# Performance work log

Hardware: AMD Instinct MI355X
Metric: run time of the kernel (lower is better)

The kernel has to match this reference:

```python
import jax, jax.numpy as jnp
import numpy as np

N_NODES = 100000
N_EDGES = 1600000
D_IN = 256
D_OUT = 256


def _init_linear(key, out_f, in_f):
    # torch nn.Linear default: U(-1/sqrt(in_f), 1/sqrt(in_f))
    kw, kb = jax.random.split(key)
    bound = 1.0 / np.sqrt(in_f)
    W = jax.random.uniform(kw, (out_f, in_f), jnp.float32, -bound, bound)
    b = jax.random.uniform(kb, (out_f,), jnp.float32, -bound, bound)
    return W, b


def setup_inputs() -> dict:
    key = jax.random.key(0)
    ks = jax.random.split(key, 7)
    x = jax.random.normal(ks[0], (N_NODES, D_IN), jnp.float32)
    edge_index = jax.random.randint(ks[1], (2, N_EDGES), 0, N_NODES, jnp.int64)
    W1, b1 = _init_linear(ks[2], D_OUT, D_IN)
    W2, b2 = _init_linear(ks[3], D_OUT // 2, D_OUT)
    W3, b3 = _init_linear(ks[4], D_OUT // 2, D_OUT)
    Wd1, bd1 = _init_linear(ks[5], D_OUT, D_OUT)
    Wd2, bd2 = _init_linear(ks[6], 1, D_OUT)
    return {"x": x, "edge_index": edge_index,
            "W1": W1, "b1": b1, "W2": W2, "b2": b2, "W3": W3, "b3": b3,
            "Wd1": Wd1, "bd1": bd1, "Wd2": Wd2, "bd2": bd2}


def _l2norm(x):
    return x / jnp.linalg.norm(x, axis=-1, keepdims=True)


def reference(x, edge_index, W1, b1, W2, b2, W3, b3, Wd1, bd1, Wd2, bd2):
    src, dst = edge_index[0], edge_index[1]  # source_to_target flow
    x = jax.nn.relu(x @ W1.T + b1)           # [N, D_OUT]
    x = _l2norm(x)
    for _ in range(2):
        # sum-aggregate neighbor messages: scatter-add x[src] into dst
        nm = jax.ops.segment_sum(x[src], dst, num_segments=N_NODES)  # [N, D_OUT]
        x = jax.nn.relu(jnp.concatenate([x @ W2.T + b2, nm @ W3.T + b3], axis=-1))
        x = _l2norm(x)
    x = jax.nn.relu(x @ Wd1.T + bd1)
    return x @ Wd2.T + bd2                    # [N, 1]
```

## Files before the change

kernel.cpp:

```cpp
#include <hip/hip_runtime.h>
#include <math.h>


typedef _Float16 f16x8 __attribute__((ext_vector_type(8)));
typedef float    f32x16 __attribute__((ext_vector_type(16)));

constexpr int DIM = 256;
constexpr int BM  = 128;
constexpr int BK  = 32;
constexpr int SA  = 40;
constexpr int SW  = 40;
constexpr int NBMAX = 392;

__device__ __forceinline__ unsigned pk_hi2(float a, float b) {
    unsigned short ha = __builtin_bit_cast(unsigned short, (_Float16)a);
    unsigned short hb = __builtin_bit_cast(unsigned short, (_Float16)b);
    return (unsigned)ha | ((unsigned)hb << 16);
}
__device__ __forceinline__ unsigned pk_lo2(float a, float b) {
    _Float16 ha = (_Float16)a, hb = (_Float16)b;
    unsigned short la = __builtin_bit_cast(unsigned short, (_Float16)(a - (float)ha));
    unsigned short lb = __builtin_bit_cast(unsigned short, (_Float16)(b - (float)hb));
    return (unsigned)la | ((unsigned)lb << 16);
}
__device__ __forceinline__ unsigned pack_pair(float v) {
    _Float16 hi = (_Float16)v;
    _Float16 lo = (_Float16)(v - (float)hi);
    return (unsigned)__builtin_bit_cast(unsigned short, hi)
         | ((unsigned)__builtin_bit_cast(unsigned short, lo) << 16);
}

template <int AMODE, int EPI>
__device__ __forceinline__
void gemm_body(const void* __restrict__ Av,
               const float* __restrict__ WA, const float* __restrict__ WB,
               const float* __restrict__ bA, const float* __restrict__ bB,
               void* __restrict__ outv,
               const float* __restrict__ wd2, const float* __restrict__ bd2,
               float* __restrict__ out1, int M)
{
    __shared__ __align__(16) _Float16 smem[30720];
    _Float16* As_hi = smem;
    _Float16* As_lo = smem + 5120;
    _Float16* Ws_hi = smem + 10240;
    _Float16* Ws_lo = smem + 20480;

    const int tid  = threadIdx.x;
    const int lane = tid & 63;
    const int w    = tid >> 6;
    const int rh   = w >> 1;
    const int ch   = w & 1;
    const int l31  = lane & 31;
    const int lh   = lane >> 5;
    const int bm0  = blockIdx.x * BM;

    const unsigned* Au = (const unsigned*)Av;
    const int srow = tid >> 3;
    const int sch  = (tid & 7) * 4;

    uint4  pa[4];
    float4 pw[8];

    auto fetchA = [&](int t) {
        const int k0 = t * BK;
        #pragma unroll
        for (int i = 0; i < 4; ++i) {
            const int gr = bm0 + srow + 32 * i;
            uint4 v = {0u, 0u, 0u, 0u};
            if (gr < M) v = *(const uint4*)&Au[(size_t)gr * 256 + k0 + sch];
            pa[i] = v;
        }
    };
    auto fetchW = [&](int t) {
        const int k0 = t * BK;
        #pragma unroll
        for (int i = 0; i < 8; ++i) {
            const int r = srow + 32 * i;
            const float* src = (r < 128) ? &WA[(size_t)r * 256]
                                         : &WB[(size_t)(r - 128) * 256];
            pw[i] = *(const float4*)&src[k0 + sch];
        }
    };
    auto stageA = [&]() {
        #pragma unroll
        for (int i = 0; i < 4; ++i) {
            const int r = srow + 32 * i;
            unsigned h0, h1, l0, l1;
            if (AMODE == 0) {
                const float x0 = __builtin_bit_cast(float, pa[i].x);
                const float x1 = __builtin_bit_cast(float, pa[i].y);
                const float x2 = __builtin_bit_cast(float, pa[i].z);
                const float x3 = __builtin_bit_cast(float, pa[i].w);
                h0 = pk_hi2(x0, x1); h1 = pk_hi2(x2, x3);
                l0 = pk_lo2(x0, x1); l1 = pk_lo2(x2, x3);
            } else {
                h0 = __builtin_amdgcn_perm(pa[i].y, pa[i].x, 0x05040100u);
                l0 = __builtin_amdgcn_perm(pa[i].y, pa[i].x, 0x07060302u);
                h1 = __builtin_amdgcn_perm(pa[i].w, pa[i].z, 0x05040100u);
                l1 = __builtin_amdgcn_perm(pa[i].w, pa[i].z, 0x07060302u);
            }
            uint2 th; th.x = h0; th.y = h1;
            uint2 tl; tl.x = l0; tl.y = l1;
            *(uint2*)&As_hi[r * SA + sch] = th;
            *(uint2*)&As_lo[r * SA + sch] = tl;
        }
    };
    auto stageW = [&]() {
        #pragma unroll
        for (int i = 0; i < 8; ++i) {
            const int r = srow + 32 * i;
            uint2 th; th.x = pk_hi2(pw[i].x, pw[i].y); th.y = pk_hi2(pw[i].z, pw[i].w);
            uint2 tl; tl.x = pk_lo2(pw[i].x, pw[i].y); tl.y = pk_lo2(pw[i].z, pw[i].w);
            *(uint2*)&Ws_hi[r * SW + sch] = th;
            *(uint2*)&Ws_lo[r * SW + sch] = tl;
        }
    };

    f32x16 acc[2][4];
    #pragma unroll
    for (int tr = 0; tr < 2; ++tr)
        #pragma unroll
        for (int tc = 0; tc < 4; ++tc)
            #pragma unroll
            for (int i = 0; i < 16; ++i) acc[tr][tc][i] = 0.0f;

    fetchA(0); fetchW(0);

    #pragma unroll 1
    for (int t = 0; t < DIM / BK; ++t) {
        stageA(); stageW();
        __syncthreads();
        if (t < DIM / BK - 1) { fetchA(t + 1); fetchW(t + 1); }

        #pragma unroll
        for (int ks = 0; ks < 2; ++ks) {
            f16x8 ah[2], al[2], wh[4], wl[4];
            #pragma unroll
            for (int tr = 0; tr < 2; ++tr) {
                const int off = (rh * 64 + tr * 32 + l31) * SA + ks * 16 + lh * 8;
                ah[tr] = *(const f16x8*)&As_hi[off];
                al[tr] = *(const f16x8*)&As_lo[off];
            }
            #pragma unroll
            for (int tc = 0; tc < 4; ++tc) {
                const int off = (ch * 128 + tc * 32 + l31) * SW + ks * 16 + lh * 8;
                wh[tc] = *(const f16x8*)&Ws_hi[off];
                wl[tc] = *(const f16x8*)&Ws_lo[off];
            }
            #pragma unroll
            for (int tr = 0; tr < 2; ++tr)
                #pragma unroll
                for (int tc = 0; tc < 4; ++tc) {
                    acc[tr][tc] = __builtin_amdgcn_mfma_f32_32x32x16_f16(ah[tr], wh[tc], acc[tr][tc], 0, 0, 0);
                    acc[tr][tc] = __builtin_amdgcn_mfma_f32_32x32x16_f16(ah[tr], wl[tc], acc[tr][tc], 0, 0, 0);
                    acc[tr][tc] = __builtin_amdgcn_mfma_f32_32x32x16_f16(al[tr], wh[tc], acc[tr][tc], 0, 0, 0);
                }
        }
        __syncthreads();
    }


    if (EPI == 0) {
        float* z = (float*)outv;
        #pragma unroll
        for (int tr = 0; tr < 2; ++tr)
            #pragma unroll
            for (int i = 0; i < 16; ++i) {
                const int r  = rh * 64 + tr * 32 + 4 * lh + (i & 3) + 8 * (i >> 2);
                const int gr = bm0 + r;
                if (gr < M) {
                    #pragma unroll
                    for (int tc = 0; tc < 4; ++tc)
                        z[(size_t)gr * 256 + ch * 128 + tc * 32 + l31] = acc[tr][tc][i];
                }
            }
        return;
    }

    {
        float bias[4];
        #pragma unroll
        for (int tc = 0; tc < 4; ++tc)
            bias[tc] = (ch ? bB : bA)[tc * 32 + l31];
        #pragma unroll
        for (int tr = 0; tr < 2; ++tr)
            #pragma unroll
            for (int tc = 0; tc < 4; ++tc)
                #pragma unroll
                for (int i = 0; i < 16; ++i)
                    acc[tr][tc][i] = fmaxf(acc[tr][tc][i] + bias[tc], 0.0f);
    }

    float* red = (float*)smem;

    if (EPI == 1) {
        float ss[2][16];
        #pragma unroll
        for (int tr = 0; tr < 2; ++tr)
            #pragma unroll
            for (int i = 0; i < 16; ++i) {
                float s = 0.f;
                #pragma unroll
                for (int tc = 0; tc < 4; ++tc) s += acc[tr][tc][i] * acc[tr][tc][i];
                #pragma unroll
                for (int m = 1; m < 32; m <<= 1) s += __shfl_xor(s, m);
                ss[tr][i] = s;
            }
        const int j  = l31;
        const int ji = j & 15, jt = j >> 4;
        red[ch * 128 + rh * 64 + jt * 32 + 4 * lh + (ji & 3) + 8 * (ji >> 2)] = ss[jt][ji];
        __syncthreads();

        unsigned* hp = (unsigned*)outv;
        #pragma unroll
        for (int tr = 0; tr < 2; ++tr)
            #pragma unroll
            for (int i = 0; i < 16; ++i) {
                const int rl = rh * 64 + tr * 32 + 4 * lh + (i & 3) + 8 * (i >> 2);
                const float inv = 1.0f / sqrtf(red[rl] + red[128 + rl]);
                const int gr = bm0 + rl;
                if (gr < M) {
                    #pragma unroll
                    for (int tc = 0; tc < 4; ++tc)
                        hp[(size_t)gr * 256 + ch * 128 + tc * 32 + l31] =
                            pack_pair(acc[tr][tc][i] * inv);
                }
            }
        return;
    }

    {
        float wv[4];
        #pragma unroll
        for (int tc = 0; tc < 4; ++tc) wv[tc] = wd2[ch * 128 + tc * 32 + l31];
        float dd[2][16];
        #pragma unroll
        for (int tr = 0; tr < 2; ++tr)
            #pragma unroll
            for (int i = 0; i < 16; ++i) {
                float s = 0.f;
                #pragma unroll
                for (int tc = 0; tc < 4; ++tc) s += acc[tr][tc][i] * wv[tc];
                #pragma unroll
                for (int m = 1; m < 32; m <<= 1) s += __shfl_xor(s, m);
                dd[tr][i] = s;
            }
        const int j  = l31;
        const int ji = j & 15, jt = j >> 4;
        red[ch * 128 + rh * 64 + jt * 32 + 4 * lh + (ji & 3) + 8 * (ji >> 2)] = dd[jt][ji];
        __syncthreads();
        if (tid < 128) {
            const int gr = bm0 + tid;
            if (gr < M) out1[gr] = red[tid] + red[128 + tid] + bd2[0];
        }
    }
}

__global__ __launch_bounds__(256, 2)
void gemm_l1(const void* __restrict__ Av,
             const float* __restrict__ WA, const float* __restrict__ WB,
             const float* __restrict__ bA, const float* __restrict__ bB,
             void* __restrict__ outv, int M, int gb,
             const int* __restrict__ ei, int E, int nb,
             int* __restrict__ gcur, int2* __restrict__ ebuf)
{
    if ((int)blockIdx.x < gb) {
        gemm_body<0, 1>(Av, WA, WB, bA, bB, outv, nullptr, nullptr, nullptr, M);
    } else {
        __shared__ int h[NBMAX], cur[NBMAX];
        const int tid = threadIdx.x;
        const int b   = (int)blockIdx.x - gb;
        for (int t = tid; t < nb; t += 256) h[t] = 0;
        __syncthreads();
        const int EB = (E + 127) >> 7;
        const int e0 = b * EB, e1 = min(E, e0 + EB);
        for (int e = e0 + tid; e < e1; e += 256)
            atomicAdd(&h[ei[E + e] >> 8], 1);
        __syncthreads();
        for (int t = tid; t < nb; t += 256)
            cur[t] = atomicAdd(&gcur[t], h[t]);
        __syncthreads();
        for (int e = e0 + tid; e < e1; e += 256) {
            const int d = ei[E + e];
            const int p = atomicAdd(&cur[d >> 8], 1);
            ebuf[p] = make_int2(d, ei[e]);
        }
    }
}

__global__ __launch_bounds__(256, 2)
void gemm_z(const void* __restrict__ Av,
            const float* __restrict__ WA, const float* __restrict__ WB,
            void* __restrict__ outv, int M)
{
    gemm_body<1, 0>(Av, WA, WB, nullptr, nullptr, outv, nullptr, nullptr, nullptr, M);
}

__global__ __launch_bounds__(256, 2)
void gemm_head(const void* __restrict__ Av,
               const float* __restrict__ WA, const float* __restrict__ WB,
               const float* __restrict__ bA, const float* __restrict__ bB,
               const float* __restrict__ wd2, const float* __restrict__ bd2,
               float* __restrict__ out1, int M)
{
    gemm_body<1, 2>(Av, WA, WB, bA, bB, nullptr, wd2, bd2, out1, M);
}


__global__ __launch_bounds__(256)
void hist_kernel(const int* __restrict__ ei, int E, int nb,
                 int* __restrict__ ghist)
{
    __shared__ int h[NBMAX];
    const int tid = threadIdx.x;
    for (int t = tid; t < nb; t += 256) h[t] = 0;
    __syncthreads();
    const int EB = (E + 127) >> 7;
    const int e0 = (int)blockIdx.x * EB, e1 = min(E, e0 + EB);
    for (int e = e0 + tid; e < e1; e += 256)
        atomicAdd(&h[ei[E + e] >> 8], 1);
    __syncthreads();
    for (int t = tid; t < nb; t += 256)
        if (h[t]) atomicAdd(&ghist[t], h[t]);
}

__global__ __launch_bounds__(512)
void scanb_kernel(const int* __restrict__ ghist, int* __restrict__ gboff,
                  int* __restrict__ gcur, int* __restrict__ rp, int M, int E,
                  int nb)
{
    __shared__ int sm[512];
    const int tid = threadIdx.x;
    const int v = (tid < nb) ? ghist[tid] : 0;
    sm[tid] = v;
    __syncthreads();
    for (int off = 1; off < 512; off <<= 1) {
        int t = (tid >= off) ? sm[tid - off] : 0;
        __syncthreads();
        sm[tid] += t;
        __syncthreads();
    }
    if (tid < nb) {
        const int ex = sm[tid] - v;
        gboff[tid] = ex;
        gcur[tid]  = ex;
    }
    if (tid == 0) { gboff[nb] = E; rp[M] = E; }
}

__global__ __launch_bounds__(256)
void bucket_kernel(const int2* __restrict__ ebuf, const int* __restrict__ gboff,
                   int* __restrict__ rp, int* __restrict__ esrc, int M)
{
    const int b   = (int)blockIdx.x;
    const int tid = threadIdx.x;
    const int base = gboff[b], top = gboff[b + 1];
    const int d0 = b << 8;
    __shared__ int c[256], sm[256], cur[256];
    c[tid] = 0;
    __syncthreads();
    for (int j = base + tid; j < top; j += 256)
        atomicAdd(&c[ebuf[j].x - d0], 1);
    __syncthreads();
    sm[tid] = c[tid];
    __syncthreads();
    for (int off = 1; off < 256; off <<= 1) {
        int t = (tid >= off) ? sm[tid - off] : 0;
        __syncthreads();
        sm[tid] += t;
        __syncthreads();
    }
    const int excl = sm[tid] - c[tid];
    const int d = d0 + tid;
    if (d < M) rp[d] = base + excl;
    cur[tid] = base + excl;
    __syncthreads();
    for (int j = base + tid; j < top; j += 256) {
        const int2 e = ebuf[j];
        const int p = atomicAdd(&cur[e.x - d0], 1);
        esrc[p] = e.y;
    }
}

__global__ __launch_bounds__(256)
void fin_kernel(const float* __restrict__ z, const int* __restrict__ rp,
                const int* __restrict__ esrc,
                const float* __restrict__ b2, const float* __restrict__ b3,
                unsigned* __restrict__ hp, int M)
{
    const int v    = blockIdx.x * 4 + (threadIdx.x >> 6);
    const int lane = threadIdx.x & 63;
    if (v >= M) return;
    const int beg = rp[v], end = rp[v + 1];
    const int deg = end - beg;

    const float2 z1 = *(const float2*)&z[(size_t)v * DIM + lane * 2];
    const float2 c2 = *(const float2*)&b2[lane * 2];
    const float2 c3 = *(const float2*)&b3[lane * 2];

    const float* z2 = z + 128;
    float ax0 = 0.f, ay0 = 0.f, ax1 = 0.f, ay1 = 0.f;
    float ax2 = 0.f, ay2 = 0.f, ax3 = 0.f, ay3 = 0.f;

    for (int base = 0; base < deg; base += 64) {
        const int cnt = min(64, deg - base);
        int myidx = 0;
        if (lane < cnt) myidx = esrc[beg + base + lane];
        int j = 0;
        for (; j + 3 < cnt; j += 4) {
            const int s0 = __builtin_amdgcn_readlane(myidx, j);
            const int s1 = __builtin_amdgcn_readlane(myidx, j + 1);
            const int s2 = __builtin_amdgcn_readlane(myidx, j + 2);
            const int s3 = __builtin_amdgcn_readlane(myidx, j + 3);
            const float2 g0 = *(const float2*)&z2[(size_t)s0 * DIM + lane * 2];
            const float2 g1 = *(const float2*)&z2[(size_t)s1 * DIM + lane * 2];
            const float2 g2 = *(const float2*)&z2[(size_t)s2 * DIM + lane * 2];
            const float2 g3 = *(const float2*)&z2[(size_t)s3 * DIM + lane * 2];
            ax0 += g0.x; ay0 += g0.y;
            ax1 += g1.x; ay1 += g1.y;
            ax2 += g2.x; ay2 += g2.y;
            ax3 += g3.x; ay3 += g3.y;
        }
        for (; j < cnt; ++j) {
            const int s0 = __builtin_amdgcn_readlane(myidx, j);
            const float2 g0 = *(const float2*)&z2[(size_t)s0 * DIM + lane * 2];
            ax0 += g0.x; ay0 += g0.y;
        }
    }
    const float sx = (ax0 + ax1) + (ax2 + ax3);
    const float sy = (ay0 + ay1) + (ay2 + ay3);

    const float u1x = fmaxf(z1.x + c2.x, 0.f), u1y = fmaxf(z1.y + c2.y, 0.f);
    const float u2x = fmaxf(sx + c3.x, 0.f),  u2y = fmaxf(sy + c3.y, 0.f);

    float ss = u1x * u1x + u1y * u1y + u2x * u2x + u2y * u2y;
    #pragma unroll
    for (int off = 32; off > 0; off >>= 1) ss += __shfl_xor(ss, off);
    const float inv = 1.0f / sqrtf(ss);

    uint2 p1; p1.x = pack_pair(u1x * inv); p1.y = pack_pair(u1y * inv);
    uint2 p2; p2.x = pack_pair(u2x * inv); p2.y = pack_pair(u2y * inv);
    *(uint2*)&hp[(size_t)v * DIM + lane * 2]       = p1;
    *(uint2*)&hp[(size_t)v * DIM + 128 + lane * 2] = p2;
}


extern "C" void kernel_launch(void* const* d_in, const int* in_sizes, int n_in,
                              void* d_out, int out_size, void* d_ws, size_t ws_size,
                              hipStream_t stream)
{
    const float* x   = (const float*)d_in[0];
    const int*   ei  = (const int*)d_in[1];
    const float* W1  = (const float*)d_in[2];
    const float* b1  = (const float*)d_in[3];
    const float* W2  = (const float*)d_in[4];
    const float* b2  = (const float*)d_in[5];
    const float* W3  = (const float*)d_in[6];
    const float* b3  = (const float*)d_in[7];
    const float* Wd1 = (const float*)d_in[8];
    const float* bd1 = (const float*)d_in[9];
    const float* Wd2 = (const float*)d_in[10];
    const float* bd2 = (const float*)d_in[11];
    float* out = (float*)d_out;

    const int M = in_sizes[0] / DIM;
    const int E = in_sizes[1] / 2;
    const int nb = (M + 255) >> 8;

    unsigned* hp  = (unsigned*)d_ws;
    float*    z   = (float*)(hp + (size_t)M * DIM);
    int*   rp     = (int*)(z + (size_t)M * DIM);
    int*   esrc   = rp + (M + 1);
    int*   ghist  = esrc + E;
    int*   gboff  = ghist + nb;
    int*   gcur   = gboff + nb + 1;
    int2*  ebuf   = (int2*)z;

    hipMemsetAsync(ghist, 0, sizeof(int) * nb, stream);

    const int gb  = (M + BM - 1) / BM;
    const int fb  = (M + 3) / 4;

    hist_kernel<<<128, 256, 0, stream>>>(ei, E, nb, ghist);
    scanb_kernel<<<1, 512, 0, stream>>>(ghist, gboff, gcur, rp, M, E, nb);

    gemm_l1<<<gb + 128, 256, 0, stream>>>(
        x, W1, W1 + 128 * DIM, b1, b1 + 128, hp, M, gb, ei, E, nb, gcur, ebuf);

    bucket_kernel<<<nb, 256, 0, stream>>>(ebuf, gboff, rp, esrc, M);

    gemm_z<<<gb, 256, 0, stream>>>(hp, W2, W3, z, M);
    fin_kernel<<<fb, 256, 0, stream>>>(z, rp, esrc, b2, b3, hp, M);

    gemm_z<<<gb, 256, 0, stream>>>(hp, W2, W3, z, M);
    fin_kernel<<<fb, 256, 0, stream>>>(z, rp, esrc, b2, b3, hp, M);

    gemm_head<<<gb, 256, 0, stream>>>(
        hp, Wd1, Wd1 + 128 * DIM, bd1, bd1 + 128, Wd2, bd2, out, M);
}
```

Measured before the change: 722.3 us.

## Prepack weights into MFMA fragment layout and stream A via global_load_lds

Adds a per-call pack kernel that splits each weight matrix into hi/lo fp16 parts laid out in MFMA fragment order, so the GEMMs read weights straight from global/L2 into registers instead of converting and staging them through LDS. The A tile is now copied into a double-buffered, XOR-swizzled LDS buffer with direct global-to-LDS loads, and the hi/lo split or conversion happens at fragment-load time. This removes the per-tile weight conversion and the LDS traffic for W, cuts LDS use, and overlaps the next stage's loads with the MFMAs. The cost is an extra launch, per-lane global weight loads that depend on L2 hits, and conversion work repeated for each fragment read.

```diff
diff --git a/kernel.cpp b/kernel.cpp
--- a/kernel.cpp
+++ b/kernel.cpp
@@ -7,22 +7,8 @@
 
 constexpr int DIM = 256;
 constexpr int BM  = 128;
-constexpr int BK  = 32;
-constexpr int SA  = 40;
-constexpr int SW  = 40;
 constexpr int NBMAX = 392;
 
-__device__ __forceinline__ unsigned pk_hi2(float a, float b) {
-    unsigned short ha = __builtin_bit_cast(unsigned short, (_Float16)a);
-    unsigned short hb = __builtin_bit_cast(unsigned short, (_Float16)b);
-    return (unsigned)ha | ((unsigned)hb << 16);
-}
-__device__ __forceinline__ unsigned pk_lo2(float a, float b) {
-    _Float16 ha = (_Float16)a, hb = (_Float16)b;
-    unsigned short la = __builtin_bit_cast(unsigned short, (_Float16)(a - (float)ha));
-    unsigned short lb = __builtin_bit_cast(unsigned short, (_Float16)(b - (float)hb));
-    return (unsigned)la | ((unsigned)lb << 16);
-}
 __device__ __forceinline__ unsigned pack_pair(float v) {
     _Float16 hi = (_Float16)v;
     _Float16 lo = (_Float16)(v - (float)hi);
@@ -30,20 +16,54 @@
          | ((unsigned)__builtin_bit_cast(unsigned short, lo) << 16);
 }
 
+__device__ __forceinline__ void glds16(const void* g, void* l) {
+    __builtin_amdgcn_global_load_lds(
+        (const __attribute__((address_space(1))) unsigned*)g,
+        (__attribute__((address_space(3))) unsigned*)l, 16, 0, 0);
+}
+
+__global__ __launch_bounds__(256)
+void pack_w_kernel(const float* __restrict__ WA0, const float* __restrict__ WB0,
+                   const float* __restrict__ WA1, const float* __restrict__ WB1,
+                   const float* __restrict__ WA2, const float* __restrict__ WB2,
+                   _Float16* __restrict__ d0, _Float16* __restrict__ d1,
+                   _Float16* __restrict__ d2)
+{
+    const int layer = (int)blockIdx.x >> 6;
+    const int tid   = ((int)blockIdx.x & 63) * 256 + threadIdx.x;
+    const float* WA = layer == 0 ? WA0 : layer == 1 ? WA1 : WA2;
+    const float* WB = layer == 0 ? WB0 : layer == 1 ? WB1 : WB2;
+    _Float16* dst   = layer == 0 ? d0  : layer == 1 ? d1  : d2;
+
+    const int lane = tid & 63;
+    const int frag = tid >> 6;
+    const int nt = frag & 7;
+    const int ks = (frag >> 3) & 1;
+    const int t  = (frag >> 4) & 7;
+    const int hl = frag >> 7;
+    const int n  = nt * 32 + (lane & 31);
+    const int k0 = t * 32 + ks * 16 + (lane >> 5) * 8;
+    const float* src = (n < 128) ? &WA[(size_t)n * 256] : &WB[(size_t)(n - 128) * 256];
+
+    f16x8 o;
+    #pragma unroll
+    for (int j = 0; j < 8; ++j) {
+        const float v = src[k0 + j];
+        const _Float16 h = (_Float16)v;
+        o[j] = hl ? (_Float16)(v - (float)h) : h;
+    }
+    *(f16x8*)&dst[(size_t)tid * 8] = o;
+}
+
 template <int AMODE, int EPI>
 __device__ __forceinline__
-void gemm_body(const void* __restrict__ Av,
-               const float* __restrict__ WA, const float* __restrict__ WB,
-               const float* __restrict__ bA, const float* __restrict__ bB,
-               void* __restrict__ outv,
-               const float* __restrict__ wd2, const float* __restrict__ bd2,
-               float* __restrict__ out1, int M)
-{
-    __shared__ __align__(16) _Float16 smem[30720];
-    _Float16* As_hi = smem;
-    _Float16* As_lo = smem + 5120;
-    _Float16* Ws_hi = smem + 10240;
-    _Float16* Ws_lo = smem + 20480;
+void gemm2_body(const void* __restrict__ Av, const _Float16* __restrict__ Wpk,
+                const float* __restrict__ bA, const float* __restrict__ bB,
+                void* __restrict__ outv,
+                const float* __restrict__ wd2, const float* __restrict__ bd2,
+                float* __restrict__ out1, int M)
+{
+    __shared__ __align__(16) unsigned smem[2][128][32];
 
     const int tid  = threadIdx.x;
     const int lane = tid & 63;
@@ -52,69 +72,14 @@
     const int ch   = w & 1;
     const int l31  = lane & 31;
     const int lh   = lane >> 5;
-    const int bm0  = blockIdx.x * BM;
-
-    const unsigned* Au = (const unsigned*)Av;
-    const int srow = tid >> 3;
-    const int sch  = (tid & 7) * 4;
-
-    uint4  pa[4];
-    float4 pw[8];
-
-    auto fetchA = [&](int t) {
-        const int k0 = t * BK;
-        #pragma unroll
-        for (int i = 0; i < 4; ++i) {
-            const int gr = bm0 + srow + 32 * i;
-            uint4 v = {0u, 0u, 0u, 0u};
-            if (gr < M) v = *(const uint4*)&Au[(size_t)gr * 256 + k0 + sch];
-            pa[i] = v;
-        }
-    };
-    auto fetchW = [&](int t) {
-        const int k0 = t * BK;
-        #pragma unroll
-        for (int i = 0; i < 8; ++i) {
-            const int r = srow + 32 * i;
-            const float* src = (r < 128) ? &WA[(size_t)r * 256]
-                                         : &WB[(size_t)(r - 128) * 256];
-            pw[i] = *(const float4*)&src[k0 + sch];
-        }
-    };
-    auto stageA = [&]() {
-        #pragma unroll
-        for (int i = 0; i < 4; ++i) {
-            const int r = srow + 32 * i;
-            unsigned h0, h1, l0, l1;
-            if (AMODE == 0) {
-                const float x0 = __builtin_bit_cast(float, pa[i].x);
-                const float x1 = __builtin_bit_cast(float, pa[i].y);
-                const float x2 = __builtin_bit_cast(float, pa[i].z);
-                const float x3 = __builtin_bit_cast(float, pa[i].w);
-                h0 = pk_hi2(x0, x1); h1 = pk_hi2(x2, x3);
-                l0 = pk_lo2(x0, x1); l1 = pk_lo2(x2, x3);
-            } else {
-                h0 = __builtin_amdgcn_perm(pa[i].y, pa[i].x, 0x05040100u);
-                l0 = __builtin_amdgcn_perm(pa[i].y, pa[i].x, 0x07060302u);
-                h1 = __builtin_amdgcn_perm(pa[i].w, pa[i].z, 0x05040100u);
-                l1 = __builtin_amdgcn_perm(pa[i].w, pa[i].z, 0x07060302u);
-            }
-            uint2 th; th.x = h0; th.y = h1;
-            uint2 tl; tl.x = l0; tl.y = l1;
-            *(uint2*)&As_hi[r * SA + sch] = th;
-            *(uint2*)&As_lo[r * SA + sch] = tl;
-        }
-    };
-    auto stageW = [&]() {
-        #pragma unroll
-        for (int i = 0; i < 8; ++i) {
-            const int r = srow + 32 * i;
-            uint2 th; th.x = pk_hi2(pw[i].x, pw[i].y); th.y = pk_hi2(pw[i].z, pw[i].w);
-            uint2 tl; tl.x = pk_lo2(pw[i].x, pw[i].y); tl.y = pk_lo2(pw[i].z, pw[i].w);
-            *(uint2*)&Ws_hi[r * SW + sch] = th;
-            *(uint2*)&Ws_lo[r * SW + sch] = tl;
-        }
-    };
+    const int bm0  = (int)blockIdx.x * BM;
+
+    const char* wh_p = (const char*)Wpk + (size_t)(ch * 4 * 64 + lane) * 16;
+    const char* wl_p = wh_p + 131072;
+
+    const int srb  = w * 32;
+    const int srow = lane >> 3;
+    const int scp  = lane & 7;
 
     f32x16 acc[2][4];
     #pragma unroll
@@ -124,40 +89,95 @@
             #pragma unroll
             for (int i = 0; i < 16; ++i) acc[tr][tc][i] = 0.0f;
 
-    fetchA(0); fetchW(0);
+    f16x8 WH0[4], WL0[4], WH1[4], WL1[4];
+
+    auto STAGE = [&](int t, int b) {
+        #pragma unroll
+        for (int i = 0; i < 4; ++i) {
+            const int r  = srb + i * 8 + srow;
+            const int rg = min(bm0 + r, M - 1);
+            const int cl = scp ^ (r & 7);
+            glds16((const char*)Av + (size_t)rg * 1024 + t * 128 + cl * 16,
+                   (void*)&smem[b][srb + i * 8][0]);
+        }
+    };
+    auto PW = [&](int s, f16x8* WH, f16x8* WL) {
+        #pragma unroll
+        for (int tc = 0; tc < 4; ++tc) {
+            WH[tc] = *(const f16x8*)(wh_p + (size_t)s * 8192 + tc * 1024);
+            WL[tc] = *(const f16x8*)(wl_p + (size_t)s * 8192 + tc * 1024);
+        }
+    };
+    auto LOADA = [&](int b, int ks, f16x8* ah, f16x8* al) {
+        #pragma unroll
+        for (int tr = 0; tr < 2; ++tr) {
+            const int r  = rh * 64 + tr * 32 + l31;
+            const int sw = r & 7;
+            const int c0 = ks * 4 + lh * 2;
+            const unsigned* Ar = &smem[b][r][0];
+            const uint4 q0 = *(const uint4*)&Ar[((c0    ) ^ sw) * 4];
+            const uint4 q1 = *(const uint4*)&Ar[((c0 + 1) ^ sw) * 4];
+            if (AMODE == 1) {
+                uint4 uh, ul;
+                uh.x = __builtin_amdgcn_perm(q0.y, q0.x, 0x05040100u);
+                uh.y = __builtin_amdgcn_perm(q0.w, q0.z, 0x05040100u);
+                uh.z = __builtin_amdgcn_perm(q1.y, q1.x, 0x05040100u);
+                uh.w = __builtin_amdgcn_perm(q1.w, q1.z, 0x05040100u);
+                ul.x = __builtin_amdgcn_perm(q0.y, q0.x, 0x07060302u);
+                ul.y = __builtin_amdgcn_perm(q0.w, q0.z, 0x07060302u);
+                ul.z = __builtin_amdgcn_perm(q1.y, q1.x, 0x07060302u);
+                ul.w = __builtin_amdgcn_perm(q1.w, q1.z, 0x07060302u);
+                ah[tr] = __builtin_bit_cast(f16x8, uh);
+                al[tr] = __builtin_bit_cast(f16x8, ul);
+            } else {
+                const float fv[8] = {
+                    __builtin_bit_cast(float, q0.x), __builtin_bit_cast(float, q0.y),
+                    __builtin_bit_cast(float, q0.z), __builtin_bit_cast(float, q0.w),
+                    __builtin_bit_cast(float, q1.x), __builtin_bit_cast(float, q1.y),
+                    __builtin_bit_cast(float, q1.z), __builtin_bit_cast(float, q1.w)};
+                #pragma unroll
+                for (int j = 0; j < 8; ++j) {
+                    const _Float16 h = (_Float16)fv[j];
+                    ah[tr][j] = h;
+                    al[tr][j] = (_Float16)(fv[j] - (float)h);
+                }
+            }
+        }
+    };
+    auto MF = [&](const f16x8* ah, const f16x8* al,
+                  const f16x8* WH, const f16x8* WL) {
+        #pragma unroll
+        for (int tr = 0; tr < 2; ++tr)
+            #pragma unroll
+            for (int tc = 0; tc < 4; ++tc) {
+                acc[tr][tc] = __builtin_amdgcn_mfma_f32_32x32x16_f16(ah[tr], WH[tc], acc[tr][tc], 0, 0, 0);
+                acc[tr][tc] = __builtin_amdgcn_mfma_f32_32x32x16_f16(ah[tr], WL[tc], acc[tr][tc], 0, 0, 0);
+                acc[tr][tc] = __builtin_amdgcn_mfma_f32_32x32x16_f16(al[tr], WH[tc], acc[tr][tc], 0, 0, 0);
+            }
+    };
+
+    STAGE(0, 0);
+    PW(0, WH0, WL0);
 
     #pragma unroll 1
-    for (int t = 0; t < DIM / BK; ++t) {
-        stageA(); stageW();
-        __syncthreads();
-        if (t < DIM / BK - 1) { fetchA(t + 1); fetchW(t + 1); }
-
-        #pragma unroll
-        for (int ks = 0; ks < 2; ++ks) {
-            f16x8 ah[2], al[2], wh[4], wl[4];
-            #pragma unroll
-            for (int tr = 0; tr < 2; ++tr) {
-                const int off = (rh * 64 + tr * 32 + l31) * SA + ks * 16 + lh * 8;
-                ah[tr] = *(const f16x8*)&As_hi[off];
-                al[tr] = *(const f16x8*)&As_lo[off];
-            }
-            #pragma unroll
-            for (int tc = 0; tc < 4; ++tc) {
-                const int off = (ch * 128 + tc * 32 + l31) * SW + ks * 16 + lh * 8;
-                wh[tc] = *(const f16x8*)&Ws_hi[off];
-                wl[tc] = *(const f16x8*)&Ws_lo[off];
-            }
-            #pragma unroll
-            for (int tr = 0; tr < 2; ++tr)
-                #pragma unroll
-                for (int tc = 0; tc < 4; ++tc) {
-                    acc[tr][tc] = __builtin_amdgcn_mfma_f32_32x32x16_f16(ah[tr], wh[tc], acc[tr][tc], 0, 0, 0);
-                    acc[tr][tc] = __builtin_amdgcn_mfma_f32_32x32x16_f16(ah[tr], wl[tc], acc[tr][tc], 0, 0, 0);
-                    acc[tr][tc] = __builtin_amdgcn_mfma_f32_32x32x16_f16(al[tr], wh[tc], acc[tr][tc], 0, 0, 0);
-                }
-        }
-        __syncthreads();
-    }
+    for (int t = 0; t < 8; ++t) {
+        __syncthreads();
+        if (t < 7) STAGE(t + 1, (t + 1) & 1);
+        const int b = t & 1;
+        {
+            if (2 * t + 1 < 16) PW(2 * t + 1, WH1, WL1);
+            f16x8 ah[2], al[2];
+            LOADA(b, 0, ah, al);
+            MF(ah, al, WH0, WL0);
+        }
+        {
+            if (2 * t + 2 < 16) PW(2 * t + 2, WH0, WL0);
+            f16x8 ah[2], al[2];
+            LOADA(b, 1, ah, al);
+            MF(ah, al, WH1, WL1);
+        }
+    }
+    __syncthreads();
 
 
     if (EPI == 0) {
@@ -257,15 +277,14 @@
 }
 
 __global__ __launch_bounds__(256, 2)
-void gemm_l1(const void* __restrict__ Av,
-             const float* __restrict__ WA, const float* __restrict__ WB,
+void gemm_l1(const void* __restrict__ Av, const _Float16* __restrict__ wpk,
              const float* __restrict__ bA, const float* __restrict__ bB,
              void* __restrict__ outv, int M, int gb,
              const int* __restrict__ ei, int E, int nb,
              int* __restrict__ gcur, int2* __restrict__ ebuf)
 {
     if ((int)blockIdx.x < gb) {
-        gemm_body<0, 1>(Av, WA, WB, bA, bB, outv, nullptr, nullptr, nullptr, M);
+        gemm2_body<0, 1>(Av, wpk, bA, bB, outv, nullptr, nullptr, nullptr, M);
     } else {
         __shared__ int h[NBMAX], cur[NBMAX];
         const int tid = threadIdx.x;
@@ -289,21 +308,19 @@
 }
 
 __global__ __launch_bounds__(256, 2)
-void gemm_z(const void* __restrict__ Av,
-            const float* __restrict__ WA, const float* __restrict__ WB,
+void gemm_z(const void* __restrict__ Av, const _Float16* __restrict__ wpk,
             void* __restrict__ outv, int M)
 {
-    gemm_body<1, 0>(Av, WA, WB, nullptr, nullptr, outv, nullptr, nullptr, nullptr, M);
+    gemm2_body<1, 0>(Av, wpk, nullptr, nullptr, outv, nullptr, nullptr, nullptr, M);
 }
 
 __global__ __launch_bounds__(256, 2)
-void gemm_head(const void* __restrict__ Av,
-               const float* __restrict__ WA, const float* __restrict__ WB,
+void gemm_head(const void* __restrict__ Av, const _Float16* __restrict__ wpk,
                const float* __restrict__ bA, const float* __restrict__ bB,
                const float* __restrict__ wd2, const float* __restrict__ bd2,
                float* __restrict__ out1, int M)
 {
-    gemm_body<1, 2>(Av, WA, WB, bA, bB, nullptr, wd2, bd2, out1, M);
+    gemm2_body<1, 2>(Av, wpk, bA, bB, nullptr, wd2, bd2, out1, M);
 }
 
 
@@ -476,25 +493,34 @@
     int*   gcur   = gboff + nb + 1;
     int2*  ebuf   = (int2*)z;
 
+    size_t woff = (size_t)((char*)(gcur + nb) - (char*)d_ws);
+    woff = (woff + 255) & ~(size_t)255;
+    _Float16* wpk1 = (_Float16*)((char*)d_ws + woff);
+    _Float16* wpk2 = wpk1 + 131072;
+    _Float16* wpkd = wpk2 + 131072;
+
     hipMemsetAsync(ghist, 0, sizeof(int) * nb, stream);
 
     const int gb  = (M + BM - 1) / BM;
     const int fb  = (M + 3) / 4;
 
+    pack_w_kernel<<<192, 256, 0, stream>>>(
+        W1, W1 + 128 * DIM, W2, W3, Wd1, Wd1 + 128 * DIM, wpk1, wpk2, wpkd);
+
     hist_kernel<<<128, 256, 0, stream>>>(ei, E, nb, ghist);
     scanb_kernel<<<1, 512, 0, stream>>>(ghist, gboff, gcur, rp, M, E, nb);
 
     gemm_l1<<<gb + 128, 256, 0, stream>>>(
-        x, W1, W1 + 128 * DIM, b1, b1 + 128, hp, M, gb, ei, E, nb, gcur, ebuf);
+        x, wpk1, b1, b1 + 128, hp, M, gb, ei, E, nb, gcur, ebuf);
 
     bucket_kernel<<<nb, 256, 0, stream>>>(ebuf, gboff, rp, esrc, M);
 
-    gemm_z<<<gb, 256, 0, stream>>>(hp, W2, W3, z, M);
+    gemm_z<<<gb, 256, 0, stream>>>(hp, wpk2, z, M);
     fin_kernel<<<fb, 256, 0, stream>>>(z, rp, esrc, b2, b3, hp, M);
 
-    gemm_z<<<gb, 256, 0, stream>>>(hp, W2, W3, z, M);
+    gemm_z<<<gb, 256, 0, stream>>>(hp, wpk2, z, M);
     fin_kernel<<<fb, 256, 0, stream>>>(z, rp, esrc, b2, b3, hp, M);
 
     gemm_head<<<gb, 256, 0, stream>>>(
-        hp, Wd1, Wd1 + 128 * DIM, bd1, bd1 + 128, Wd2, bd2, out, M);
-}
+        hp, wpkd, bd1, bd1 + 128, Wd2, bd2, out, M);
+}
```

Result: no change. 716.6 us (-0.8%).
